# Performance work log

Measured on AMD Instinct MI355X. Metric: run time of the kernel, lower is better.

Reference implementation:

```python
import jax, jax.numpy as jnp
import numpy as np

NEG_SLOPE = 0.01  # torch leaky_relu default

def _lrelu(x):
    return jax.nn.leaky_relu(x, NEG_SLOPE)

def _l2norm(x, axis):
    # torch F.normalize(p=2, eps=1e-12)
    n = jnp.linalg.norm(x, axis=axis, keepdims=True)
    return x / jnp.maximum(n, 1e-12)

def setup_inputs() -> dict:
    key = jax.random.key(0)
    ks = jax.random.split(key, 12)
    Nda, Nq, C, Din, Dout = 10000, 64, 1024, 128, 256
    target_adj = (jax.random.uniform(ks[0], (Nda, Nda)) < 0.002).astype(jnp.float32)
    query_adj = (jax.random.uniform(ks[1], (Nq, Nq)) < 0.2).astype(jnp.float32)
    node_features_da = jax.random.normal(ks[2], (Nda, Din), dtype=jnp.float32)
    node_features_q = jax.random.normal(ks[3], (Nq, Din), dtype=jnp.float32)
    candidate_set = jax.random.randint(ks[4], (C,), 0, Nda)
    candidate_adj = (jax.random.uniform(ks[5], (C, C)) < 0.01).astype(jnp.float32)
    s_in = 1.0 / np.sqrt(Din).astype(np.float32)
    s_out = 1.0 / np.sqrt(Dout).astype(np.float32)
    W1_da = jax.random.normal(ks[6], (Din, Dout), dtype=jnp.float32) * s_in
    W1_q = jax.random.normal(ks[7], (Din, Dout), dtype=jnp.float32) * s_in
    W2_da = jax.random.normal(ks[8], (Dout, Dout), dtype=jnp.float32) * s_out
    W2_q = jax.random.normal(ks[9], (Dout, Dout), dtype=jnp.float32) * s_out
    threshold = jnp.float32(0.2)
    return {"target_adj": target_adj, "node_features_da": node_features_da,
            "query_adj": query_adj, "node_features_q": node_features_q,
            "candidate_set": candidate_set, "candidate_adj": candidate_adj,
            "threshold": threshold, "W1_da": W1_da, "W1_q": W1_q,
            "W2_da": W2_da, "W2_q": W2_q}

def _cross_cosine(q, da, candidate_set):
    # cosine similarity between each query node and each candidate target node: [Nq, C]
    return _l2norm(q, 1) @ _l2norm(da[candidate_set], 1).T

def reference(target_adj, node_features_da, query_adj, node_features_q,
              candidate_set, candidate_adj, threshold, W1_da, W1_q, W2_da, W2_q):
    # layer 1: GCN propagation on both graphs (gcn(adj,x) = adj @ x @ W)
    da1 = _lrelu(target_adj @ (node_features_da @ W1_da))   # [Nda, D]
    q1 = _lrelu(query_adj @ (node_features_q @ W1_q))       # [Nq, D]
    c1 = _cross_cosine(q1, da1, candidate_set)               # [Nq, C]
    pre_da1 = da1[candidate_set]                             # [C, D]
    # NOTE: da1[candidate_set].data = ... mutates a temporary in torch -> no-op on da1
    att_da1 = _lrelu(da1)                                    # dropout in eval = identity
    h1_q = c1 @ pre_da1                                      # [Nq, D]
    att_q1 = _lrelu(q1 + _l2norm(h1_q, 0))
    # layer 2
    da2 = _lrelu(target_adj @ (att_da1 @ W2_da))
    q2 = _lrelu(query_adj @ (att_q1 @ W2_q))
    c2 = _cross_cosine(q2, da2, candidate_set)
    pre_da2 = da2[candidate_set]
    att_da2 = _lrelu(da2)                                    # in-place update is again a no-op
    h2_q = c2 @ pre_da2
    att_q2 = _lrelu(q2 + _l2norm(h2_q, 0))
    # graph-level matching score per target node
    emb = jnp.mean(att_q2, axis=0, keepdims=True)            # [1, D]
    num = att_da2 @ emb[0]                                   # [Nda]
    den = jnp.maximum(jnp.linalg.norm(att_da2, axis=1) * jnp.linalg.norm(emb), 1e-8)
    end = (num / den)[None, :]                               # [1, Nda]
    # threshold selection expressed with a mask (jit-safe, same math: excluded
    # rows/cols are zero and do not affect L2 norms, sums, or the trace)
    m = (end[0] > threshold).astype(att_da2.dtype)           # [Nda]
    F_ = att_da2 * m[:, None]
    re_adj = F_ @ F_.T                                       # [Nda, Nda]
    nor_re = _l2norm(re_adj, 1) * target_adj                 # elementwise with original adj
    cnt = jnp.sum(m)
    total = jnp.sum(nor_re)
    tr = jnp.trace(nor_re)
    has = cnt > 0
    pre_avg_degree = jnp.where(has, total / jnp.maximum(cnt, 1.0), 0.0)
    pre_avg_nodes = jnp.where(has, tr, 0.0)
    pre_density = jnp.where(has, 2.0 * total / (tr * (tr - 1.0) + 1e-4), 0.0)
    return (end, att_da2, att_q2, pre_avg_degree, pre_density, pre_avg_nodes)
```

## Files before the change

kernel.cpp:

```cpp
#include <hip/hip_runtime.h>

constexpr int NDA = 10000;
constexpr int NQ  = 64;
constexpr int CND = 1024;
constexpr int DIN = 128;
constexpr int D   = 256;
constexpr int CAP = 96;
constexpr int NB_BIG = ((NDA + 63) / 64) * (D / 64);

#define LRELU(x) ((x) >= 0.f ? (x) : 0.01f * (x))

__device__ __forceinline__ float wave_red64(float v) {
#pragma unroll
    for (int o = 32; o; o >>= 1) v += __shfl_down(v, o);
    return v;
}

struct GemmSmem { float As[32][68]; float Bs[32][68]; };

template <bool RELU_A, bool RELU_C>
__device__ __forceinline__ void gemm_body(GemmSmem& sm, int bx, int by,
                                          const float* __restrict__ A,
                                          const float* __restrict__ B,
                                          float* __restrict__ C,
                                          int M, int N, int K) {
    const int bm = bx * 64, bn = by * 64;
    const int tid = threadIdx.x;
    const int tx = tid & 15, ty = tid >> 4;
    const int lm = tid >> 2, lk = (tid & 3) * 8;
    const int kb = tid >> 3, nb = (tid & 7) * 8;
    const bool aValid = (bm + lm) < M;
    const float* aPtr = A + (size_t)(bm + lm) * K + lk;
    const float* bPtr = B + (size_t)kb * N + bn + nb;
    float4 ra0 = make_float4(0.f, 0.f, 0.f, 0.f), ra1 = ra0, rb0, rb1;
    if (aValid) { ra0 = *(const float4*)aPtr; ra1 = *(const float4*)(aPtr + 4); }
    rb0 = *(const float4*)bPtr;
    rb1 = *(const float4*)(bPtr + 4);
    float acc[4][4] = {};
    for (int k0 = 0; k0 < K; k0 += 32) {
        float4 wa0 = ra0, wa1 = ra1, wb0 = rb0, wb1 = rb1;
        if (RELU_A) {
            wa0.x = LRELU(wa0.x); wa0.y = LRELU(wa0.y); wa0.z = LRELU(wa0.z); wa0.w = LRELU(wa0.w);
            wa1.x = LRELU(wa1.x); wa1.y = LRELU(wa1.y); wa1.z = LRELU(wa1.z); wa1.w = LRELU(wa1.w);
        }
        sm.As[lk + 0][lm] = wa0.x; sm.As[lk + 1][lm] = wa0.y;
        sm.As[lk + 2][lm] = wa0.z; sm.As[lk + 3][lm] = wa0.w;
        sm.As[lk + 4][lm] = wa1.x; sm.As[lk + 5][lm] = wa1.y;
        sm.As[lk + 6][lm] = wa1.z; sm.As[lk + 7][lm] = wa1.w;
        *(float4*)&sm.Bs[kb][nb]     = wb0;
        *(float4*)&sm.Bs[kb][nb + 4] = wb1;
        __syncthreads();
        if (k0 + 32 < K) {
            if (aValid) {
                ra0 = *(const float4*)(aPtr + k0 + 32);
                ra1 = *(const float4*)(aPtr + k0 + 36);
            }
            rb0 = *(const float4*)(bPtr + (size_t)(k0 + 32) * N);
            rb1 = *(const float4*)(bPtr + (size_t)(k0 + 32) * N + 4);
        }
#pragma unroll
        for (int kk = 0; kk < 32; kk++) {
            float av[4], bv[4];
#pragma unroll
            for (int i = 0; i < 4; i++) av[i] = sm.As[kk][ty * 4 + i];
#pragma unroll
            for (int j = 0; j < 4; j++) bv[j] = sm.Bs[kk][tx * 4 + j];
#pragma unroll
            for (int i = 0; i < 4; i++)
#pragma unroll
                for (int j = 0; j < 4; j++) acc[i][j] += av[i] * bv[j];
        }
        __syncthreads();
    }
#pragma unroll
    for (int i = 0; i < 4; i++) {
        int r = bm + ty * 4 + i;
        if (r < M) {
            float4 v = make_float4(acc[i][0], acc[i][1], acc[i][2], acc[i][3]);
            if (RELU_C) { v.x = LRELU(v.x); v.y = LRELU(v.y); v.z = LRELU(v.z); v.w = LRELU(v.w); }
            *(float4*)(C + (size_t)r * N + bn + tx * 4) = v;
        }
    }
}

__device__ __forceinline__ void csr_body(const float* __restrict__ adj,
                                         int* __restrict__ cols,
                                         int* __restrict__ rowcnt, int row) {
    __shared__ int scnt;
    if (threadIdx.x == 0) scnt = 0;
    __syncthreads();
    const float4* rp = (const float4*)(adj + (size_t)row * NDA);
    for (int i = threadIdx.x; i < NDA / 4; i += 256) {
        float4 v = rp[i];
        if (v.x != 0.f) { int s = atomicAdd(&scnt, 1); if (s < CAP) cols[row * CAP + s] = 4 * i; }
        if (v.y != 0.f) { int s = atomicAdd(&scnt, 1); if (s < CAP) cols[row * CAP + s] = 4 * i + 1; }
        if (v.z != 0.f) { int s = atomicAdd(&scnt, 1); if (s < CAP) cols[row * CAP + s] = 4 * i + 2; }
        if (v.w != 0.f) { int s = atomicAdd(&scnt, 1); if (s < CAP) cols[row * CAP + s] = 4 * i + 3; }
    }
    __syncthreads();
    if (threadIdx.x == 0) rowcnt[row] = min(scnt, CAP);
}

__device__ __forceinline__ void spmm_body(const int* __restrict__ cols,
                                          const int* __restrict__ rowcnt,
                                          const float* __restrict__ X,
                                          float* __restrict__ out1,
                                          float* __restrict__ out2, int row) {
    int d = threadIdx.x;
    int cnt = rowcnt[row];
    __shared__ int sc[CAP];
    if (d < cnt) sc[d] = cols[row * CAP + d];
    __syncthreads();
    float a0 = 0.f, a1 = 0.f, a2 = 0.f, a3 = 0.f;
    int k = 0;
    for (; k + 4 <= cnt; k += 4) {
        a0 += X[(size_t)sc[k + 0] * D + d];
        a1 += X[(size_t)sc[k + 1] * D + d];
        a2 += X[(size_t)sc[k + 2] * D + d];
        a3 += X[(size_t)sc[k + 3] * D + d];
    }
    for (; k < cnt; k++) a0 += X[(size_t)sc[k] * D + d];
    float v = LRELU(a0 + a1 + a2 + a3);
    out1[(size_t)row * D + d] = v;
    if (out2) out2[(size_t)row * D + d] = LRELU(v);
}

__global__ __launch_bounds__(256) void stage0_kernel(const float* __restrict__ adj,
                                                     int* __restrict__ cols,
                                                     int* __restrict__ rowcnt,
                                                     const float* __restrict__ Fda,
                                                     const float* __restrict__ W1da,
                                                     float* __restrict__ X1,
                                                     const float* __restrict__ Fq,
                                                     const float* __restrict__ W1q,
                                                     float* __restrict__ Xq) {
    __shared__ GemmSmem gs;
    int bid = blockIdx.x;
    if (bid < NB_BIG) {
        gemm_body<false, false>(gs, bid >> 2, bid & 3, Fda, W1da, X1, NDA, D, DIN);
    } else if (bid < NB_BIG + 4) {
        gemm_body<false, false>(gs, 0, bid - NB_BIG, Fq, W1q, Xq, NQ, D, DIN);
    } else {
        csr_body(adj, cols, rowcnt, bid - (NB_BIG + 4));
    }
}

__global__ __launch_bounds__(256) void stage_sg_kernel(const int* __restrict__ cols,
                                                       const int* __restrict__ rowcnt,
                                                       const float* __restrict__ X,
                                                       float* __restrict__ out1,
                                                       float* __restrict__ out2,
                                                       const float* __restrict__ Aq,
                                                       const float* __restrict__ Bq,
                                                       float* __restrict__ Cq) {
    __shared__ GemmSmem gs;
    int bid = blockIdx.x;
    if (bid < 4) {
        gemm_body<false, true>(gs, 0, bid, Aq, Bq, Cq, NQ, D, NQ);
    } else {
        spmm_body(cols, rowcnt, X, out1, out2, bid - 4);
    }
}

__global__ __launch_bounds__(256) void stage4_kernel(const float* __restrict__ da1,
                                                     const float* __restrict__ W2da,
                                                     float* __restrict__ Y2,
                                                     const float* __restrict__ aq1,
                                                     const float* __restrict__ W2q,
                                                     float* __restrict__ Zq) {
    __shared__ GemmSmem gs;
    int bid = blockIdx.x;
    if (bid < NB_BIG) {
        gemm_body<true, false>(gs, bid >> 2, bid & 3, da1, W2da, Y2, NDA, D, D);
    } else {
        gemm_body<false, false>(gs, 0, bid - NB_BIG, aq1, W2q, Zq, NQ, D, D);
    }
}

__global__ __launch_bounds__(256) void gemmH_kernel(const float* __restrict__ A,
                                                    const float* __restrict__ B,
                                                    float* __restrict__ C) {
    __shared__ GemmSmem gs;
    gemm_body<false, false>(gs, blockIdx.x, blockIdx.y, A, B, C, NDA, D, D);
}

__global__ __launch_bounds__(256) void cross_kernel(const float* __restrict__ q,
                                                    const float* __restrict__ da,
                                                    const int* __restrict__ cand,
                                                    float* __restrict__ hpart) {
    __shared__ float qs[D];
    __shared__ float cmw[256];
    __shared__ int sci[256];
    __shared__ float red[4];
    __shared__ float sqn;
    int r = blockIdx.x, qr = blockIdx.y;
    int d = threadIdx.x;
    float qv = q[r * D + d];
    qs[d] = qv;
    sci[d] = cand[qr * 256 + d];
    float p = wave_red64(qv * qv);
    int w = d >> 6, lane = d & 63;
    if (lane == 0) red[w] = p;
    __syncthreads();
    if (d == 0) sqn = fmaxf(sqrtf(red[0] + red[1] + red[2] + red[3]), 1e-12f);
    __syncthreads();
    float qn = sqn;
    {
        const float4* ap = (const float4*)(da + (size_t)sci[d] * D);
        float dot = 0.f, sq = 0.f;
#pragma unroll 8
        for (int k = 0; k < D / 4; k++) {
            float4 v = ap[k];
            dot += qs[4 * k] * v.x + qs[4 * k + 1] * v.y + qs[4 * k + 2] * v.z + qs[4 * k + 3] * v.w;
            sq  += v.x * v.x + v.y * v.y + v.z * v.z + v.w * v.w;
        }
        cmw[d] = dot / (qn * fmaxf(sqrtf(sq), 1e-12f));
    }
    __syncthreads();
    float a0 = 0.f, a1 = 0.f, a2 = 0.f, a3 = 0.f, a4 = 0.f, a5 = 0.f, a6 = 0.f, a7 = 0.f;
    for (int c = 0; c < 256; c += 8) {
        a0 += cmw[c + 0] * da[(size_t)sci[c + 0] * D + d];
        a1 += cmw[c + 1] * da[(size_t)sci[c + 1] * D + d];
        a2 += cmw[c + 2] * da[(size_t)sci[c + 2] * D + d];
        a3 += cmw[c + 3] * da[(size_t)sci[c + 3] * D + d];
        a4 += cmw[c + 4] * da[(size_t)sci[c + 4] * D + d];
        a5 += cmw[c + 5] * da[(size_t)sci[c + 5] * D + d];
        a6 += cmw[c + 6] * da[(size_t)sci[c + 6] * D + d];
        a7 += cmw[c + 7] * da[(size_t)sci[c + 7] * D + d];
    }
    hpart[((size_t)qr * NQ + r) * D + d] = ((a0 + a1) + (a2 + a3)) + ((a4 + a5) + (a6 + a7));
}

__global__ __launch_bounds__(256) void attq_kernel(const float* __restrict__ q,
                                                   const float* __restrict__ hpart,
                                                   float* __restrict__ attq,
                                                   float* __restrict__ emb) {
    int d = threadIdx.x;
    float hv[NQ];
    float ss = 0.f;
#pragma unroll
    for (int r = 0; r < NQ; r++) {
        float h = hpart[(size_t)r * D + d]
                + hpart[(size_t)(NQ + r) * D + d]
                + hpart[(size_t)(2 * NQ + r) * D + d]
                + hpart[(size_t)(3 * NQ + r) * D + d];
        hv[r] = h;
        ss += h * h;
    }
    float inv = 1.f / fmaxf(sqrtf(ss), 1e-12f);
    float es = 0.f;
#pragma unroll
    for (int r = 0; r < NQ; r++) {
        float v = q[r * D + d] + hv[r] * inv;
        v = LRELU(v);
        attq[r * D + d] = v;
        es += v;
    }
    if (emb) {
        float e = es * (1.f / (float)NQ);
        emb[d] = e;
        float p = wave_red64(e * e);
        __shared__ float red[4];
        int w = d >> 6, lane = d & 63;
        if (lane == 0) red[w] = p;
        __syncthreads();
        if (d == 0) emb[D] = sqrtf(red[0] + red[1] + red[2] + red[3]);
    }
}

__global__ __launch_bounds__(256) void end_kernel(const float* __restrict__ A,
                                                  const float* __restrict__ emb,
                                                  const float* __restrict__ thr_p,
                                                  float* __restrict__ endv,
                                                  float* __restrict__ m,
                                                  float* __restrict__ cnt) {
    __shared__ float se[D];
    __shared__ float scnt;
    int d = threadIdx.x;
    se[d] = emb[d];
    if (d == 0) scnt = 0.f;
    __syncthreads();
    float embn = emb[D];
    float thr = *thr_p;
    int w = d >> 6, lane = d & 63;
    int row = blockIdx.x * 4 + w;
    const float* ar = A + (size_t)row * D;
    float num = 0.f, sq = 0.f;
#pragma unroll
    for (int s = 0; s < 4; s++) {
        float v = ar[lane + 64 * s];
        num += v * se[lane + 64 * s];
        sq += v * v;
    }
#pragma unroll
    for (int o = 32; o; o >>= 1) { num += __shfl_down(num, o); sq += __shfl_down(sq, o); }
    if (lane == 0) {
        float den = fmaxf(sqrtf(sq) * embn, 1e-8f);
        float e = num / den;
        endv[row] = e;
        float mv = e > thr ? 1.f : 0.f;
        m[row] = mv;
        if (mv != 0.f) atomicAdd(&scnt, 1.f);
    }
    __syncthreads();
    if (d == 0 && scnt != 0.f) atomicAdd(cnt, scnt);
}

constexpr int GCHUNK = 400;
__global__ __launch_bounds__(256) void G_kernel(const float* __restrict__ A,
                                                const float* __restrict__ m,
                                                float* __restrict__ G) {
    __shared__ float SA[8][64], SB[8][64];
    int ti = blockIdx.x >> 2, tj = blockIdx.x & 3;
    int base = blockIdx.y * GCHUNK;
    int tid = threadIdx.x;
    int tx = tid & 15, ty = tid >> 4;
    float acc[4][4] = {};
    for (int g0 = 0; g0 < GCHUNK; g0 += 8) {
        for (int l = tid; l < 512; l += 256) {
            int rr = l >> 6, c = l & 63;
            int r = base + g0 + rr;
            float mv = m[r];
            SA[rr][c] = A[(size_t)r * D + ti * 64 + c] * mv;
            SB[rr][c] = A[(size_t)r * D + tj * 64 + c];
        }
        __syncthreads();
#pragma unroll
        for (int rr = 0; rr < 8; rr++) {
            float av[4], bv[4];
#pragma unroll
            for (int i = 0; i < 4; i++) av[i] = SA[rr][ty * 4 + i];
#pragma unroll
            for (int j = 0; j < 4; j++) bv[j] = SB[rr][tx * 4 + j];
#pragma unroll
            for (int i = 0; i < 4; i++)
#pragma unroll
                for (int j = 0; j < 4; j++) acc[i][j] += av[i] * bv[j];
        }
        __syncthreads();
    }
#pragma unroll
    for (int i = 0; i < 4; i++)
#pragma unroll
        for (int j = 0; j < 4; j++)
            atomicAdd(&G[(ti * 64 + ty * 4 + i) * D + tj * 64 + tx * 4 + j], acc[i][j]);
}

__global__ __launch_bounds__(256) void final_kernel(const int* __restrict__ cols,
                                                    const int* __restrict__ rowcnt,
                                                    const float* __restrict__ m,
                                                    const float* __restrict__ A,
                                                    const float* __restrict__ H,
                                                    double* __restrict__ total,
                                                    double* __restrict__ tr) {
    int i = blockIdx.x;
    if (m[i] == 0.f) return;
    int d = threadIdx.x;
    int cnt = rowcnt[i];
    __shared__ int sc[CAP];
    __shared__ float smask[CAP];
    __shared__ int sdiag;
    __shared__ float r1[4], r2[4], r3[4];
    if (d == 0) sdiag = 0;
    if (d < cnt) {
        int j = cols[i * CAP + d];
        sc[d] = j;
        smask[d] = m[j];
        if (j == i) sdiag = 1;
    }
    __syncthreads();
    float av = A[(size_t)i * D + d];
    float hv = H[(size_t)i * D + d];
    float sd = 0.f;
    for (int k = 0; k < cnt; k++)
        if (smask[k] != 0.f) sd += A[(size_t)sc[k] * D + d];
    float p1 = av * sd, p2 = av * hv, p3 = av * av;
#pragma unroll
    for (int o = 32; o; o >>= 1) {
        p1 += __shfl_down(p1, o);
        p2 += __shfl_down(p2, o);
        p3 += __shfl_down(p3, o);
    }
    int w = d >> 6, lane = d & 63;
    if (lane == 0) { r1[w] = p1; r2[w] = p2; r3[w] = p3; }
    __syncthreads();
    if (d == 0) {
        float num  = r1[0] + r1[1] + r1[2] + r1[3];
        float den2 = r2[0] + r2[1] + r2[2] + r2[3];
        float self = r3[0] + r3[1] + r3[2] + r3[3];
        float denom = fmaxf(sqrtf(den2), 1e-12f);
        double inv = 1.0 / (double)denom;
        if (num != 0.f) atomicAdd(total, (double)num * inv);
        if (sdiag) atomicAdd(tr, (double)self * inv);
    }
}

__global__ void scalars_kernel(const float* __restrict__ cnt,
                               const double* __restrict__ total,
                               const double* __restrict__ tr,
                               float* __restrict__ out) {
    float c = *cnt;
    float T = (float)*total;
    float R = (float)*tr;
    bool has = c > 0.f;
    out[0] = has ? (T / fmaxf(c, 1.f)) : 0.f;
    out[1] = has ? (2.f * T / (R * (R - 1.f) + 1e-4f)) : 0.f;
    out[2] = has ? R : 0.f;
}

extern "C" void kernel_launch(void* const* d_in, const int* in_sizes, int n_in,
                              void* d_out, int out_size, void* d_ws, size_t ws_size,
                              hipStream_t stream) {
    (void)in_sizes; (void)n_in; (void)out_size; (void)ws_size;
    const float* adj  = (const float*)d_in[0];
    const float* Fda  = (const float*)d_in[1];
    const float* Qadj = (const float*)d_in[2];
    const float* Fq   = (const float*)d_in[3];
    const int*   cand = (const int*)d_in[4];
    const float* thr  = (const float*)d_in[6];
    const float* W1da = (const float*)d_in[7];
    const float* W1q  = (const float*)d_in[8];
    const float* W2da = (const float*)d_in[9];
    const float* W2q  = (const float*)d_in[10];

    float* out = (float*)d_out;
    float* o_end    = out;
    float* o_attda2 = out + NDA;
    float* o_attq2  = out + NDA + (size_t)NDA * D;
    float* o_sc     = o_attq2 + NQ * D;

    char* w = (char*)d_ws;
    size_t off = 0;
    auto alloc = [&](size_t b) { size_t r = off; off += (b + 255) & ~(size_t)255; return r; };
    float* bufA = (float*)(w + alloc((size_t)NDA * D * 4));
    float* bufB = (float*)(w + alloc((size_t)NDA * D * 4));
    float* bufC = (float*)(w + alloc((size_t)NDA * D * 4));
    int* colsb   = (int*)(w + alloc((size_t)NDA * CAP * 4));
    int* rowcntb = (int*)(w + alloc((size_t)NDA * 4));
    float* mbuf  = (float*)(w + alloc((size_t)NDA * 4));
    char* zbase = w + alloc(262144 + 256);
    float* Gb    = (float*)zbase;
    float* cntb  = (float*)(zbase + 262144);
    double* totb = (double*)(zbase + 262144 + 8);
    double* trb  = (double*)(zbase + 262144 + 16);
    float* xq   = (float*)(w + alloc((size_t)NQ * D * 4));
    float* q1b  = (float*)(w + alloc((size_t)NQ * D * 4));
    float* aq1  = (float*)(w + alloc((size_t)NQ * D * 4));
    float* q2b  = (float*)(w + alloc((size_t)NQ * D * 4));
    float* hpart = (float*)(w + alloc((size_t)4 * NQ * D * 4));
    float* embb = (float*)(w + alloc((size_t)(D + 1) * 4));

    hipMemsetAsync(zbase, 0, 262144 + 256, stream);

    stage0_kernel<<<NB_BIG + 4 + NDA, 256, 0, stream>>>(adj, colsb, rowcntb,
                                                        Fda, W1da, bufA,
                                                        Fq, W1q, xq);
    stage_sg_kernel<<<NDA + 4, 256, 0, stream>>>(colsb, rowcntb, bufA, bufB, (float*)nullptr,
                                                 Qadj, xq, q1b);
    cross_kernel<<<dim3(NQ, 4), 256, 0, stream>>>(q1b, bufB, cand, hpart);
    attq_kernel<<<1, 256, 0, stream>>>(q1b, hpart, aq1, (float*)nullptr);
    stage4_kernel<<<NB_BIG + 4, 256, 0, stream>>>(bufB, W2da, bufA, aq1, W2q, xq);
    stage_sg_kernel<<<NDA + 4, 256, 0, stream>>>(colsb, rowcntb, bufA, bufC, o_attda2,
                                                 Qadj, xq, q2b);
    cross_kernel<<<dim3(NQ, 4), 256, 0, stream>>>(q2b, bufC, cand, hpart);
    attq_kernel<<<1, 256, 0, stream>>>(q2b, hpart, o_attq2, embb);
    end_kernel<<<NDA / 4, 256, 0, stream>>>(o_attda2, embb, thr, o_end, mbuf, cntb);
    G_kernel<<<dim3(16, NDA / GCHUNK), 256, 0, stream>>>(o_attda2, mbuf, Gb);
    gemmH_kernel<<<dim3((NDA + 63) / 64, D / 64), 256, 0, stream>>>(o_attda2, Gb, bufB);
    final_kernel<<<NDA, 256, 0, stream>>>(colsb, rowcntb, mbuf, o_attda2, bufB, totb, trb);
    scalars_kernel<<<1, 1, 0, stream>>>(cntb, totb, trb, o_sc);
}
```

Measured before the change: 1.050 ms.

## Co-schedule cross with W2 GEMM, fuse attq into Zq GEMM, deterministic G reduction

The first cross-similarity step now runs in the same launch as the large da1·W2 GEMM, since the two are independent. The attq computation is fused into a small kernel that also computes the query-side W2 product. The G = Fᵀ·A accumulation now writes per-chunk partials that a separate kernel sums, replacing float atomics and the large memset. This removes launches and atomic contention, at the cost of an extra partial buffer and one more small reduction kernel. The qfused kernel recomputes the hpart reduction in each of its 4 blocks.

```diff
diff --git a/kernel.cpp b/kernel.cpp
--- a/kernel.cpp
+++ b/kernel.cpp
@@ -125,6 +125,53 @@
     if (out2) out2[(size_t)row * D + d] = LRELU(v);
 }
 
+__device__ __forceinline__ void cross_body(const float* __restrict__ q,
+                                           const float* __restrict__ da,
+                                           const int* __restrict__ cand,
+                                           float* __restrict__ hpart,
+                                           int r, int qr) {
+    __shared__ float qs[D];
+    __shared__ float cmw[256];
+    __shared__ int sci[256];
+    __shared__ float red[4];
+    __shared__ float sqn;
+    int d = threadIdx.x;
+    float qv = q[r * D + d];
+    qs[d] = qv;
+    sci[d] = cand[qr * 256 + d];
+    float p = wave_red64(qv * qv);
+    int w = d >> 6, lane = d & 63;
+    if (lane == 0) red[w] = p;
+    __syncthreads();
+    if (d == 0) sqn = fmaxf(sqrtf(red[0] + red[1] + red[2] + red[3]), 1e-12f);
+    __syncthreads();
+    float qn = sqn;
+    {
+        const float4* ap = (const float4*)(da + (size_t)sci[d] * D);
+        float dot = 0.f, sq = 0.f;
+#pragma unroll 8
+        for (int k = 0; k < D / 4; k++) {
+            float4 v = ap[k];
+            dot += qs[4 * k] * v.x + qs[4 * k + 1] * v.y + qs[4 * k + 2] * v.z + qs[4 * k + 3] * v.w;
+            sq  += v.x * v.x + v.y * v.y + v.z * v.z + v.w * v.w;
+        }
+        cmw[d] = dot / (qn * fmaxf(sqrtf(sq), 1e-12f));
+    }
+    __syncthreads();
+    float a0 = 0.f, a1 = 0.f, a2 = 0.f, a3 = 0.f, a4 = 0.f, a5 = 0.f, a6 = 0.f, a7 = 0.f;
+    for (int c = 0; c < 256; c += 8) {
+        a0 += cmw[c + 0] * da[(size_t)sci[c + 0] * D + d];
+        a1 += cmw[c + 1] * da[(size_t)sci[c + 1] * D + d];
+        a2 += cmw[c + 2] * da[(size_t)sci[c + 2] * D + d];
+        a3 += cmw[c + 3] * da[(size_t)sci[c + 3] * D + d];
+        a4 += cmw[c + 4] * da[(size_t)sci[c + 4] * D + d];
+        a5 += cmw[c + 5] * da[(size_t)sci[c + 5] * D + d];
+        a6 += cmw[c + 6] * da[(size_t)sci[c + 6] * D + d];
+        a7 += cmw[c + 7] * da[(size_t)sci[c + 7] * D + d];
+    }
+    hpart[((size_t)qr * NQ + r) * D + d] = ((a0 + a1) + (a2 + a3)) + ((a4 + a5) + (a6 + a7));
+}
+
 __global__ __launch_bounds__(256) void stage0_kernel(const float* __restrict__ adj,
                                                      int* __restrict__ cols,
                                                      int* __restrict__ rowcnt,
@@ -162,73 +209,83 @@
     }
 }
 
-__global__ __launch_bounds__(256) void stage4_kernel(const float* __restrict__ da1,
+__global__ __launch_bounds__(256) void mergeA_kernel(const float* __restrict__ q1,
+                                                     const float* __restrict__ da1,
+                                                     const int* __restrict__ cand,
+                                                     float* __restrict__ hpart,
                                                      const float* __restrict__ W2da,
-                                                     float* __restrict__ Y2,
-                                                     const float* __restrict__ aq1,
-                                                     const float* __restrict__ W2q,
-                                                     float* __restrict__ Zq) {
-    __shared__ GemmSmem gs;
+                                                     float* __restrict__ Y2) {
     int bid = blockIdx.x;
-    if (bid < NB_BIG) {
-        gemm_body<true, false>(gs, bid >> 2, bid & 3, da1, W2da, Y2, NDA, D, D);
+    if (bid < 256) {
+        cross_body(q1, da1, cand, hpart, bid >> 2, bid & 3);
     } else {
-        gemm_body<false, false>(gs, 0, bid - NB_BIG, aq1, W2q, Zq, NQ, D, D);
-    }
-}
-
-__global__ __launch_bounds__(256) void gemmH_kernel(const float* __restrict__ A,
-                                                    const float* __restrict__ B,
-                                                    float* __restrict__ C) {
-    __shared__ GemmSmem gs;
-    gemm_body<false, false>(gs, blockIdx.x, blockIdx.y, A, B, C, NDA, D, D);
+        __shared__ GemmSmem gs;
+        int b = bid - 256;
+        gemm_body<true, false>(gs, b >> 2, b & 3, da1, W2da, Y2, NDA, D, D);
+    }
 }
 
 __global__ __launch_bounds__(256) void cross_kernel(const float* __restrict__ q,
                                                     const float* __restrict__ da,
                                                     const int* __restrict__ cand,
                                                     float* __restrict__ hpart) {
-    __shared__ float qs[D];
-    __shared__ float cmw[256];
-    __shared__ int sci[256];
-    __shared__ float red[4];
-    __shared__ float sqn;
-    int r = blockIdx.x, qr = blockIdx.y;
+    cross_body(q, da, cand, hpart, blockIdx.x, blockIdx.y);
+}
+
+__global__ __launch_bounds__(256) void qfused_kernel(const float* __restrict__ q,
+                                                     const float* __restrict__ hpart,
+                                                     const float* __restrict__ W2q,
+                                                     float* __restrict__ Zq) {
+    __shared__ float aqT[D][68];
+    __shared__ float Bs[32][68];
     int d = threadIdx.x;
-    float qv = q[r * D + d];
-    qs[d] = qv;
-    sci[d] = cand[qr * 256 + d];
-    float p = wave_red64(qv * qv);
-    int w = d >> 6, lane = d & 63;
-    if (lane == 0) red[w] = p;
-    __syncthreads();
-    if (d == 0) sqn = fmaxf(sqrtf(red[0] + red[1] + red[2] + red[3]), 1e-12f);
-    __syncthreads();
-    float qn = sqn;
-    {
-        const float4* ap = (const float4*)(da + (size_t)sci[d] * D);
-        float dot = 0.f, sq = 0.f;
-#pragma unroll 8
-        for (int k = 0; k < D / 4; k++) {
-            float4 v = ap[k];
-            dot += qs[4 * k] * v.x + qs[4 * k + 1] * v.y + qs[4 * k + 2] * v.z + qs[4 * k + 3] * v.w;
-            sq  += v.x * v.x + v.y * v.y + v.z * v.z + v.w * v.w;
-        }
-        cmw[d] = dot / (qn * fmaxf(sqrtf(sq), 1e-12f));
-    }
-    __syncthreads();
-    float a0 = 0.f, a1 = 0.f, a2 = 0.f, a3 = 0.f, a4 = 0.f, a5 = 0.f, a6 = 0.f, a7 = 0.f;
-    for (int c = 0; c < 256; c += 8) {
-        a0 += cmw[c + 0] * da[(size_t)sci[c + 0] * D + d];
-        a1 += cmw[c + 1] * da[(size_t)sci[c + 1] * D + d];
-        a2 += cmw[c + 2] * da[(size_t)sci[c + 2] * D + d];
-        a3 += cmw[c + 3] * da[(size_t)sci[c + 3] * D + d];
-        a4 += cmw[c + 4] * da[(size_t)sci[c + 4] * D + d];
-        a5 += cmw[c + 5] * da[(size_t)sci[c + 5] * D + d];
-        a6 += cmw[c + 6] * da[(size_t)sci[c + 6] * D + d];
-        a7 += cmw[c + 7] * da[(size_t)sci[c + 7] * D + d];
-    }
-    hpart[((size_t)qr * NQ + r) * D + d] = ((a0 + a1) + (a2 + a3)) + ((a4 + a5) + (a6 + a7));
+    float hv[NQ];
+    float ss = 0.f;
+#pragma unroll
+    for (int r = 0; r < NQ; r++) {
+        float h = hpart[(size_t)r * D + d]
+                + hpart[(size_t)(NQ + r) * D + d]
+                + hpart[(size_t)(2 * NQ + r) * D + d]
+                + hpart[(size_t)(3 * NQ + r) * D + d];
+        hv[r] = h;
+        ss += h * h;
+    }
+    float inv = 1.f / fmaxf(sqrtf(ss), 1e-12f);
+#pragma unroll
+    for (int r = 0; r < NQ; r++) {
+        float v = q[r * D + d] + hv[r] * inv;
+        aqT[d][r] = LRELU(v);
+    }
+    __syncthreads();
+    const int bn = blockIdx.x * 64;
+    const int tx = d & 15, ty = d >> 4;
+    const int kb = d >> 3, nb = (d & 7) * 8;
+    float acc[4][4] = {};
+    for (int k0 = 0; k0 < D; k0 += 32) {
+        float4 b0 = *(const float4*)(W2q + (size_t)(k0 + kb) * D + bn + nb);
+        float4 b1 = *(const float4*)(W2q + (size_t)(k0 + kb) * D + bn + nb + 4);
+        *(float4*)&Bs[kb][nb]     = b0;
+        *(float4*)&Bs[kb][nb + 4] = b1;
+        __syncthreads();
+#pragma unroll
+        for (int kk = 0; kk < 32; kk++) {
+            float av[4], bv[4];
+#pragma unroll
+            for (int i = 0; i < 4; i++) av[i] = aqT[k0 + kk][ty * 4 + i];
+#pragma unroll
+            for (int j = 0; j < 4; j++) bv[j] = Bs[kk][tx * 4 + j];
+#pragma unroll
+            for (int i = 0; i < 4; i++)
+#pragma unroll
+                for (int j = 0; j < 4; j++) acc[i][j] += av[i] * bv[j];
+        }
+        __syncthreads();
+    }
+#pragma unroll
+    for (int i = 0; i < 4; i++) {
+        float4 v = make_float4(acc[i][0], acc[i][1], acc[i][2], acc[i][3]);
+        *(float4*)(Zq + (size_t)(ty * 4 + i) * D + bn + tx * 4) = v;
+    }
 }
 
 __global__ __launch_bounds__(256) void attq_kernel(const float* __restrict__ q,
@@ -306,10 +363,11 @@
     if (d == 0 && scnt != 0.f) atomicAdd(cnt, scnt);
 }
 
-constexpr int GCHUNK = 400;
-__global__ __launch_bounds__(256) void G_kernel(const float* __restrict__ A,
-                                                const float* __restrict__ m,
-                                                float* __restrict__ G) {
+constexpr int NCHUNK = 16;
+constexpr int GCHUNK = 640;
+__global__ __launch_bounds__(256) void Gpart_kernel(const float* __restrict__ A,
+                                                    const float* __restrict__ m,
+                                                    float* __restrict__ Gp) {
     __shared__ float SA[8][64], SB[8][64];
     int ti = blockIdx.x >> 2, tj = blockIdx.x & 3;
     int base = blockIdx.y * GCHUNK;
@@ -320,9 +378,14 @@
         for (int l = tid; l < 512; l += 256) {
             int rr = l >> 6, c = l & 63;
             int r = base + g0 + rr;
-            float mv = m[r];
-            SA[rr][c] = A[(size_t)r * D + ti * 64 + c] * mv;
-            SB[rr][c] = A[(size_t)r * D + tj * 64 + c];
+            float av = 0.f, bv = 0.f, mv = 0.f;
+            if (r < NDA) {
+                mv = m[r];
+                av = A[(size_t)r * D + ti * 64 + c];
+                bv = A[(size_t)r * D + tj * 64 + c];
+            }
+            SA[rr][c] = av * mv;
+            SB[rr][c] = bv;
         }
         __syncthreads();
 #pragma unroll
@@ -339,11 +402,28 @@
         }
         __syncthreads();
     }
+    float* gp = Gp + (size_t)blockIdx.y * D * D;
 #pragma unroll
     for (int i = 0; i < 4; i++)
 #pragma unroll
         for (int j = 0; j < 4; j++)
-            atomicAdd(&G[(ti * 64 + ty * 4 + i) * D + tj * 64 + tx * 4 + j], acc[i][j]);
+            gp[(ti * 64 + ty * 4 + i) * D + tj * 64 + tx * 4 + j] = acc[i][j];
+}
+
+__global__ __launch_bounds__(256) void Gred_kernel(const float* __restrict__ Gp,
+                                                   float* __restrict__ G) {
+    int idx = blockIdx.x * 256 + threadIdx.x;
+    float s = 0.f;
+#pragma unroll
+    for (int c = 0; c < NCHUNK; c++) s += Gp[(size_t)c * D * D + idx];
+    G[idx] = s;
+}
+
+__global__ __launch_bounds__(256) void gemmH_kernel(const float* __restrict__ A,
+                                                    const float* __restrict__ B,
+                                                    float* __restrict__ C) {
+    __shared__ GemmSmem gs;
+    gemm_body<false, false>(gs, blockIdx.x, blockIdx.y, A, B, C, NDA, D, D);
 }
 
 __global__ __launch_bounds__(256) void final_kernel(const int* __restrict__ cols,
@@ -438,34 +518,34 @@
     int* colsb   = (int*)(w + alloc((size_t)NDA * CAP * 4));
     int* rowcntb = (int*)(w + alloc((size_t)NDA * 4));
     float* mbuf  = (float*)(w + alloc((size_t)NDA * 4));
-    char* zbase = w + alloc(262144 + 256);
-    float* Gb    = (float*)zbase;
-    float* cntb  = (float*)(zbase + 262144);
-    double* totb = (double*)(zbase + 262144 + 8);
-    double* trb  = (double*)(zbase + 262144 + 16);
+    float* Gb    = (float*)(w + alloc((size_t)D * D * 4));
+    float* Gp    = (float*)(w + alloc((size_t)NCHUNK * D * D * 4));
+    char* zbase = w + alloc(256);
+    float* cntb  = (float*)zbase;
+    double* totb = (double*)(zbase + 8);
+    double* trb  = (double*)(zbase + 16);
     float* xq   = (float*)(w + alloc((size_t)NQ * D * 4));
     float* q1b  = (float*)(w + alloc((size_t)NQ * D * 4));
-    float* aq1  = (float*)(w + alloc((size_t)NQ * D * 4));
     float* q2b  = (float*)(w + alloc((size_t)NQ * D * 4));
     float* hpart = (float*)(w + alloc((size_t)4 * NQ * D * 4));
     float* embb = (float*)(w + alloc((size_t)(D + 1) * 4));
 
-    hipMemsetAsync(zbase, 0, 262144 + 256, stream);
+    hipMemsetAsync(zbase, 0, 256, stream);
 
     stage0_kernel<<<NB_BIG + 4 + NDA, 256, 0, stream>>>(adj, colsb, rowcntb,
                                                         Fda, W1da, bufA,
                                                         Fq, W1q, xq);
     stage_sg_kernel<<<NDA + 4, 256, 0, stream>>>(colsb, rowcntb, bufA, bufB, (float*)nullptr,
                                                  Qadj, xq, q1b);
-    cross_kernel<<<dim3(NQ, 4), 256, 0, stream>>>(q1b, bufB, cand, hpart);
-    attq_kernel<<<1, 256, 0, stream>>>(q1b, hpart, aq1, (float*)nullptr);
-    stage4_kernel<<<NB_BIG + 4, 256, 0, stream>>>(bufB, W2da, bufA, aq1, W2q, xq);
+    mergeA_kernel<<<256 + NB_BIG, 256, 0, stream>>>(q1b, bufB, cand, hpart, W2da, bufA);
+    qfused_kernel<<<4, 256, 0, stream>>>(q1b, hpart, W2q, xq);
     stage_sg_kernel<<<NDA + 4, 256, 0, stream>>>(colsb, rowcntb, bufA, bufC, o_attda2,
                                                  Qadj, xq, q2b);
     cross_kernel<<<dim3(NQ, 4), 256, 0, stream>>>(q2b, bufC, cand, hpart);
     attq_kernel<<<1, 256, 0, stream>>>(q2b, hpart, o_attq2, embb);
     end_kernel<<<NDA / 4, 256, 0, stream>>>(o_attda2, embb, thr, o_end, mbuf, cntb);
-    G_kernel<<<dim3(16, NDA / GCHUNK), 256, 0, stream>>>(o_attda2, mbuf, Gb);
+    Gpart_kernel<<<dim3(16, NCHUNK), 256, 0, stream>>>(o_attda2, mbuf, Gp);
+    Gred_kernel<<<D * D / 256, 256, 0, stream>>>(Gp, Gb);
     gemmH_kernel<<<dim3((NDA + 63) / 64, D / 64), 256, 0, stream>>>(o_attda2, Gb, bufB);
     final_kernel<<<NDA, 256, 0, stream>>>(colsb, rowcntb, mbuf, o_attda2, bufB, totb, trb);
     scalars_kernel<<<1, 1, 0, stream>>>(cntb, totb, trb, o_sc);
```

Result: no change. 1.060 ms (+1.0%).
